# Kernel optimization log

Hardware: AMD Instinct MI355X
Metric: run time of the kernel (lower is better)

Reference implementation:

```python
import jax, jax.numpy as jnp
import numpy as np

V, D = 1_000_000, 128
N0, N1, N2 = 1_048_576, 131_072, 16_384
E0, E1, EP = 1_048_576, 131_072, 16_384


def setup_inputs() -> dict:
    key = jax.random.key(0)
    ks = jax.random.split(key, 20)
    inp = {
        'emb': jax.random.normal(ks[0], (V, D), jnp.float32) * 0.1,
        'bias': jnp.zeros((V, 1), jnp.float32),
        'nids': jax.random.randint(ks[1], (N0,), 0, V),
        'src0': jax.random.randint(ks[2], (E0,), 0, N0),
        'dst0': jax.random.randint(ks[3], (E0,), 0, N1),
        'w0': jax.random.uniform(ks[4], (E0,), jnp.float32),
        'src1': jax.random.randint(ks[5], (E1,), 0, N1),
        'dst1': jax.random.randint(ks[6], (E1,), 0, N2),
        'w1': jax.random.uniform(ks[7], (E1,), jnp.float32),
        'pos_src': jax.random.randint(ks[8], (EP,), 0, N2),
        'pos_dst': jax.random.randint(ks[9], (EP,), 0, N2),
        'neg_src': jax.random.randint(ks[10], (EP,), 0, N2),
        'neg_dst': jax.random.randint(ks[11], (EP,), 0, N2),
        'Q0w': jax.random.normal(ks[12], (D, D), jnp.float32) / np.sqrt(D),
        'Q0b': jnp.zeros((D,), jnp.float32),
        'W0w': jax.random.normal(ks[13], (2 * D, D), jnp.float32) / np.sqrt(2 * D),
        'W0b': jnp.zeros((D,), jnp.float32),
        'Q1w': jax.random.normal(ks[14], (D, D), jnp.float32) / np.sqrt(D),
        'Q1b': jnp.zeros((D,), jnp.float32),
        'W1w': jax.random.normal(ks[15], (2 * D, D), jnp.float32) / np.sqrt(2 * D),
        'W1b': jnp.zeros((D,), jnp.float32),
    }
    return inp


def _sage_conv(h_src, h_dst, src, dst, w, Qw, Qb, Ww, Wb, n_dst):
    # n = relu(Q h_src); m = sum_e w_e * n[src_e] per dst; ws = sum_e w_e per dst
    n = jax.nn.relu(h_src @ Qw + Qb)                                   # [N_src, H]
    m = jax.ops.segment_sum(n[src] * w[:, None], dst, num_segments=n_dst)
    ws = jnp.clip(jax.ops.segment_sum(w, dst, num_segments=n_dst), 1.0, None)[:, None]
    z = jax.nn.relu(jnp.concatenate([m / ws, h_dst], axis=1) @ Ww + Wb)
    zn = jnp.linalg.norm(z, axis=1, keepdims=True)
    return z / jnp.where(zn == 0, 1.0, zn)


def _pair_score(h, bias_nid, src, dst):
    # u_dot_v + bias_src + bias_dst  -> [E, 1]
    s = jnp.sum(h[src] * h[dst], axis=1, keepdims=True)
    return s + bias_nid[src] + bias_nid[dst]


def reference(emb, bias, nids, src0, dst0, w0, src1, dst1, w1,
              pos_src, pos_dst, neg_src, neg_dst,
              Q0w, Q0b, W0w, W0b, Q1w, Q1b, W1w, W1b):
    h = emb[nids]                                                      # [N0, D]
    h1 = _sage_conv(h, h[:N1], src0, dst0, w0, Q0w, Q0b, W0w, W0b, N1)  # [N1, D]
    h2 = _sage_conv(h1, h1[:N2], src1, dst1, w1, Q1w, Q1b, W1w, W1b, N2)  # [N2, D]
    h_item = emb[nids[:N2]] + h2                                       # [N2, D]
    bias_nid = bias[nids[:N2]]                                         # [N2, 1]
    pos = _pair_score(h_item, bias_nid, pos_src, pos_dst)
    neg = _pair_score(h_item, bias_nid, neg_src, neg_dst)
    return jax.nn.relu(neg - pos + 1.0)                                # [EP, 1]
```

## Files before the change

### kernel.cpp

```cpp
#include <hip/hip_runtime.h>
#include <stdint.h>

#define V_SZ   1000000
#define N0_SZ  1048576
#define N1_SZ  131072
#define N2_SZ  16384
#define E0_SZ  1048576
#define E1_SZ  131072
#define EP_SZ  16384

typedef short bf16x8 __attribute__((ext_vector_type(8)));
typedef float f32x4  __attribute__((ext_vector_type(4)));

__device__ __forceinline__ unsigned short f2bf(float f) {
  union { float f; unsigned u; } v; v.f = f;
  unsigned r = v.u + 0x7FFFu + ((v.u >> 16) & 1u);
  return (unsigned short)(r >> 16);
}
__device__ __forceinline__ float bf2f(unsigned short h) {
  union { unsigned u; float f; } v; v.u = ((unsigned)h) << 16;
  return v.f;
}
__device__ __forceinline__ unsigned pack2bf(float a, float b) {
  return ((unsigned)f2bf(b) << 16) | (unsigned)f2bf(a);
}

__global__ __launch_bounds__(256) void prepw_all_k(
    const float* __restrict__ Q0w, const float* __restrict__ W0w,
    const float* __restrict__ Q1w, const float* __restrict__ W1w,
    unsigned short* __restrict__ Q0T, unsigned short* __restrict__ W0T,
    unsigned short* __restrict__ Q1T, unsigned short* __restrict__ W1T) {
  int t = blockIdx.x * 256 + threadIdx.x;
  const float* W; unsigned short* WT; int K; int base;
  if (t < 16384)      { W = Q0w; WT = Q0T; K = 128; base = 0; }
  else if (t < 49152) { W = W0w; WT = W0T; K = 256; base = 16384; }
  else if (t < 65536) { W = Q1w; WT = Q1T; K = 128; base = 49152; }
  else                { W = W1w; WT = W1T; K = 256; base = 65536; }
  int u = t - base;
  int n = u & 127, k = u >> 7;
  WT[(size_t)n * K + k] = f2bf(W[u]);
}

__global__ __launch_bounds__(256) void hist_all_k(const int* __restrict__ dst0,
                                                  const int* __restrict__ dst1,
                                                  int* __restrict__ counts) {
  int e = blockIdx.x * 256 + threadIdx.x;
  if (e < E0_SZ) atomicAdd(&counts[dst0[e]], 1);
  else if (e < E0_SZ + E1_SZ) atomicAdd(&counts[N1_SZ + dst1[e - E0_SZ]], 1);
}

__global__ __launch_bounds__(256) void scan_bsums_k(const int* __restrict__ counts,
                                                    int* __restrict__ bsums) {
  __shared__ int red[256];
  int base = blockIdx.x * 1024, t = threadIdx.x;
  int s = 0;
  #pragma unroll
  for (int i = 0; i < 4; i++) s += counts[base + t * 4 + i];
  red[t] = s;
  __syncthreads();
  for (int st = 128; st > 0; st >>= 1) {
    if (t < st) red[t] += red[t + st];
    __syncthreads();
  }
  if (t == 0) bsums[blockIdx.x] = red[0];
}

__global__ __launch_bounds__(256) void scan_top2_k(int* __restrict__ bsums,
                                                   int* __restrict__ offs0_last,
                                                   int* __restrict__ offs1_last) {
  __shared__ int lds[256];
  int b = blockIdx.x, t = threadIdx.x;
  int nb = (b == 0) ? 128 : 16;
  int off = (b == 0) ? 0 : 128;
  int v = (t < nb) ? bsums[off + t] : 0;
  lds[t] = v;
  __syncthreads();
  for (int st = 1; st < 256; st <<= 1) {
    int x = (t >= st) ? lds[t - st] : 0;
    __syncthreads();
    lds[t] += x;
    __syncthreads();
  }
  if (t < nb) bsums[off + t] = lds[t] - v;
  if (t == nb - 1) *((b == 0) ? offs0_last : offs1_last) = lds[t];
}

__global__ __launch_bounds__(256) void scan_final_k(const int* __restrict__ counts,
                                                    const int* __restrict__ bsums,
                                                    int* __restrict__ offs0,
                                                    int* __restrict__ offs1) {
  __shared__ int tsum[256];
  int b = blockIdx.x, t = threadIdx.x;
  int base = b * 1024;
  int v0 = counts[base + t * 4 + 0], v1 = counts[base + t * 4 + 1];
  int v2 = counts[base + t * 4 + 2], v3 = counts[base + t * 4 + 3];
  int s = v0 + v1 + v2 + v3;
  tsum[t] = s;
  __syncthreads();
  for (int st = 1; st < 256; st <<= 1) {
    int x = (t >= st) ? tsum[t - st] : 0;
    __syncthreads();
    tsum[t] += x;
    __syncthreads();
  }
  int pre = bsums[b] + tsum[t] - s;
  int* op = (b < 128) ? (offs0 + base) : (offs1 + base - N1_SZ);
  op[t * 4 + 0] = pre;
  op[t * 4 + 1] = pre + v0;
  op[t * 4 + 2] = pre + v0 + v1;
  op[t * 4 + 3] = pre + v0 + v1 + v2;
}

__global__ __launch_bounds__(256) void scatter_all_k(
    const int* __restrict__ src0, const int* __restrict__ dst0, const float* __restrict__ w0,
    const int* __restrict__ src1, const int* __restrict__ dst1, const float* __restrict__ w1,
    const int* __restrict__ offs0, const int* __restrict__ offs1,
    int* __restrict__ cursor,
    int2* __restrict__ esw0, int* __restrict__ edst0,
    int2* __restrict__ esw1, int* __restrict__ edst1) {
  int e = blockIdx.x * 256 + threadIdx.x;
  if (e < E0_SZ) {
    int d = dst0[e];
    int p = offs0[d] + atomicAdd(&cursor[d], 1);
    esw0[p] = make_int2(src0[e], __float_as_int(w0[e]));
    edst0[p] = d;
  } else if (e < E0_SZ + E1_SZ) {
    int ee = e - E0_SZ;
    int d = dst1[ee];
    int p = offs1[d] + atomicAdd(&cursor[N1_SZ + d], 1);
    esw1[p] = make_int2(src1[ee], __float_as_int(w1[ee]));
    edst1[p] = d;
  }
}

#define AM_GATHER 0
#define AM_BF16   1
#define AM_F32DIV 2
#define EPI_BF16        0
#define EPI_NORM        1
#define EPI_NORM_ADDEMB 2

template <int KCHUNKS, int AM0, int AM1, int EPI>
__global__ __launch_bounds__(256) void gemm_k(const void* __restrict__ asrc0,
                                              const void* __restrict__ asrc1,
                                              const int* __restrict__ ids,
                                              const unsigned short* __restrict__ BT,
                                              const float* __restrict__ biasv,
                                              void* __restrict__ outp,
                                              const float* __restrict__ emb,
                                              const float* __restrict__ wsumv) {
  __shared__ unsigned short lA[64][136];
  __shared__ unsigned short lB[128][136];
  const int tid = threadIdx.x;
  const int lane = tid & 63;
  const int wid = tid >> 6;
  const int rowbase = blockIdx.x * 64;
  const int Ktot = KCHUNKS * 128;

  f32x4 acc[8];
  #pragma unroll
  for (int i = 0; i < 8; i++) acc[i] = (f32x4){0.f, 0.f, 0.f, 0.f};

  for (int c = 0; c < KCHUNKS; ++c) {
    if (c) __syncthreads();
    const int am = (c == 0) ? AM0 : AM1;
    const void* asrc = (c == 0) ? asrc0 : asrc1;
    if (am == AM_GATHER) {
      const float* fsrc = (const float*)asrc;
      #pragma unroll
      for (int i = 0; i < 8; i++) {
        int f = i * 256 + tid;
        int r = f >> 5, c4 = f & 31;
        const float* rp = fsrc + (size_t)ids[rowbase + r] * 128;
        float4 v = *(const float4*)(rp + c4 * 4);
        uint2 pk;
        pk.x = pack2bf(v.x, v.y);
        pk.y = pack2bf(v.z, v.w);
        *(uint2*)(&lA[r][c4 * 4]) = pk;
      }
    } else if (am == AM_F32DIV) {
      const float* fsrc = (const float*)asrc;
      #pragma unroll
      for (int i = 0; i < 8; i++) {
        int f = i * 256 + tid;
        int r = f >> 5, c4 = f & 31;
        int row = rowbase + r;
        float inv = 1.0f / fmaxf(wsumv[row], 1.0f);
        const float* rp = fsrc + (size_t)row * 128;
        float4 v = *(const float4*)(rp + c4 * 4);
        uint2 pk;
        pk.x = pack2bf(v.x * inv, v.y * inv);
        pk.y = pack2bf(v.z * inv, v.w * inv);
        *(uint2*)(&lA[r][c4 * 4]) = pk;
      }
    } else {
      const unsigned short* bsrc = (const unsigned short*)asrc;
      #pragma unroll
      for (int i = 0; i < 4; i++) {
        int f = i * 256 + tid;
        int r = f >> 4, c8 = f & 15;
        uint4 v = *(const uint4*)(bsrc + (size_t)(rowbase + r) * 128 + c8 * 8);
        *(uint4*)(&lA[r][c8 * 8]) = v;
      }
    }
    {
      const unsigned short* bp = BT + c * 128;
      #pragma unroll
      for (int i = 0; i < 8; i++) {
        int f = i * 256 + tid;
        int n = f >> 4, c8 = f & 15;
        uint4 v = *(const uint4*)(bp + (size_t)n * Ktot + c8 * 8);
        *(uint4*)(&lB[n][c8 * 8]) = v;
      }
    }
    __syncthreads();

    const int mr = wid * 16 + (lane & 15);
    const int kq = (lane >> 4) * 8;
    #pragma unroll
    for (int kk = 0; kk < 128; kk += 32) {
      bf16x8 af = *(const bf16x8*)(&lA[mr][kk + kq]);
      #pragma unroll
      for (int nt = 0; nt < 8; ++nt) {
        bf16x8 bfr = *(const bf16x8*)(&lB[nt * 16 + (lane & 15)][kk + kq]);
        acc[nt] = __builtin_amdgcn_mfma_f32_16x16x32_bf16(af, bfr, acc[nt], 0, 0, 0);
      }
    }
  }

  const int crow = wid * 16 + ((lane >> 4) << 2);
  float vreg[8][4];
  #pragma unroll
  for (int nt = 0; nt < 8; ++nt) {
    int col = nt * 16 + (lane & 15);
    float b = biasv[col];
    #pragma unroll
    for (int r = 0; r < 4; ++r) {
      float v = acc[nt][r] + b;
      vreg[nt][r] = v > 0.f ? v : 0.f;
    }
  }
  if (EPI == EPI_BF16) {
    unsigned short* op = (unsigned short*)outp;
    #pragma unroll
    for (int nt = 0; nt < 8; ++nt) {
      int col = nt * 16 + (lane & 15);
      #pragma unroll
      for (int r = 0; r < 4; ++r)
        op[(size_t)(rowbase + crow + r) * 128 + col] = f2bf(vreg[nt][r]);
    }
  } else {
    float ss[4] = {0.f, 0.f, 0.f, 0.f};
    #pragma unroll
    for (int nt = 0; nt < 8; ++nt)
      #pragma unroll
      for (int r = 0; r < 4; ++r) ss[r] += vreg[nt][r] * vreg[nt][r];
    #pragma unroll
    for (int r = 0; r < 4; ++r) {
      ss[r] += __shfl_xor(ss[r], 1);
      ss[r] += __shfl_xor(ss[r], 2);
      ss[r] += __shfl_xor(ss[r], 4);
      ss[r] += __shfl_xor(ss[r], 8);
    }
    float sc[4];
    #pragma unroll
    for (int r = 0; r < 4; ++r) sc[r] = ss[r] > 0.f ? rsqrtf(ss[r]) : 1.0f;
    if (EPI == EPI_NORM) {
      unsigned short* op = (unsigned short*)outp;
      #pragma unroll
      for (int nt = 0; nt < 8; ++nt) {
        int col = nt * 16 + (lane & 15);
        #pragma unroll
        for (int r = 0; r < 4; ++r)
          op[(size_t)(rowbase + crow + r) * 128 + col] = f2bf(vreg[nt][r] * sc[r]);
      }
    } else {
      float* op = (float*)outp;
      #pragma unroll
      for (int nt = 0; nt < 8; ++nt) {
        int col = nt * 16 + (lane & 15);
        #pragma unroll
        for (int r = 0; r < 4; ++r) {
          int row = rowbase + crow + r;
          op[(size_t)row * 128 + col] =
              vreg[nt][r] * sc[r] + emb[(size_t)ids[row] * 128 + col];
        }
      }
    }
  }
}

template <int LAYER>
__global__ __launch_bounds__(256) void eqagg_k(
    const float* __restrict__ embf,
    const unsigned short* __restrict__ hsrc,
    const int* __restrict__ nids,
    const int2* __restrict__ esw,
    const int* __restrict__ edst,
    const unsigned short* __restrict__ BT,
    const float* __restrict__ biasv,
    float* __restrict__ aoutf,
    float* __restrict__ wsumf) {
  constexpr int ETOT = (LAYER == 0) ? E0_SZ : E1_SZ;
  __shared__ unsigned short lA[64][136];
  __shared__ unsigned short lB[128][136];
  __shared__ float lw[64];
  __shared__ int ldst[64];
  const int tid = threadIdx.x;
  const int lane = tid & 63;
  const int wid = tid >> 6;
  const int base0 = blockIdx.x * 64;

  #pragma unroll
  for (int i = 0; i < 8; i++) {
    int f = i * 256 + tid;
    int n = f >> 4, c8 = f & 15;
    *(uint4*)(&lB[n][c8 * 8]) = *(const uint4*)(BT + (size_t)n * 128 + c8 * 8);
  }
  if (tid < 64) {
    int2 sw = esw[base0 + tid];
    lw[tid] = __int_as_float(sw.y);
    ldst[tid] = edst[base0 + tid];
  }
  if (LAYER == 0) {
    #pragma unroll
    for (int i = 0; i < 8; i++) {
      int f = i * 256 + tid;
      int r = f >> 5, c4 = f & 31;
      int s = esw[base0 + r].x;
      const float* rp = embf + (size_t)nids[s] * 128;
      float4 v = *(const float4*)(rp + c4 * 4);
      uint2 pk;
      pk.x = pack2bf(v.x, v.y);
      pk.y = pack2bf(v.z, v.w);
      *(uint2*)(&lA[r][c4 * 4]) = pk;
    }
  } else {
    #pragma unroll
    for (int i = 0; i < 4; i++) {
      int f = i * 256 + tid;
      int r = f >> 4, c8 = f & 15;
      int s = esw[base0 + r].x;
      *(uint4*)(&lA[r][c8 * 8]) = *(const uint4*)(hsrc + (size_t)s * 128 + c8 * 8);
    }
  }
  __syncthreads();

  const int mr = wid * 16 + (lane & 15);
  const int kq = (lane >> 4) * 8;
  f32x4 acc[8];
  #pragma unroll
  for (int i = 0; i < 8; i++) acc[i] = (f32x4){0.f, 0.f, 0.f, 0.f};
  #pragma unroll
  for (int kk = 0; kk < 128; kk += 32) {
    bf16x8 af = *(const bf16x8*)(&lA[mr][kk + kq]);
    #pragma unroll
    for (int nt = 0; nt < 8; ++nt) {
      bf16x8 bfr = *(const bf16x8*)(&lB[nt * 16 + (lane & 15)][kk + kq]);
      acc[nt] = __builtin_amdgcn_mfma_f32_16x16x32_bf16(af, bfr, acc[nt], 0, 0, 0);
    }
  }
  const int crow = wid * 16 + ((lane >> 4) << 2);
  #pragma unroll
  for (int nt = 0; nt < 8; ++nt) {
    int col = nt * 16 + (lane & 15);
    float b = biasv[col];
    #pragma unroll
    for (int r = 0; r < 4; ++r) {
      float v = acc[nt][r] + b;
      lA[crow + r][col] = f2bf(v > 0.f ? v : 0.f);
    }
  }

  const int r0 = wid * 16;
  const int prevd = (wid > 0) ? ldst[r0 - 1]
                              : (base0 > 0 ? edst[base0 - 1] : -1);
  const int nextd = (wid < 3) ? ldst[r0 + 16]
                              : (base0 + 64 < ETOT ? edst[base0 + 64] : -1);
  float ax = 0.f, ay = 0.f, wa = 0.f;
  int cur = ldst[r0];
  int rstart = 0;
  #pragma unroll
  for (int rr = 0; rr < 16; ++rr) {
    int d = ldst[r0 + rr];
    if (d != cur) {
      bool interior = (rstart > 0 || prevd != cur);
      float* rowp = aoutf + (size_t)cur * 128 + lane * 2;
      if (interior) {
        rowp[0] = ax; rowp[1] = ay;
        if (lane == 0) wsumf[cur] = wa;
      } else {
        atomicAdd(rowp, ax); atomicAdd(rowp + 1, ay);
        if (lane == 0) atomicAdd(&wsumf[cur], wa);
      }
      ax = ay = wa = 0.f;
      cur = d;
      rstart = rr;
    }
    float w = lw[r0 + rr];
    unsigned u = *(const unsigned*)(&lA[r0 + rr][lane * 2]);
    ax += w * bf2f((unsigned short)(u & 0xffffu));
    ay += w * bf2f((unsigned short)(u >> 16));
    wa += w;
  }
  {
    bool interior = (rstart > 0 || prevd != cur) && (nextd != cur);
    float* rowp = aoutf + (size_t)cur * 128 + lane * 2;
    if (interior) {
      rowp[0] = ax; rowp[1] = ay;
      if (lane == 0) wsumf[cur] = wa;
    } else {
      atomicAdd(rowp, ax); atomicAdd(rowp + 1, ay);
      if (lane == 0) atomicAdd(&wsumf[cur], wa);
    }
  }
}

__global__ __launch_bounds__(256) void score_k(const float* __restrict__ hitem,
                                               const float* __restrict__ bias,
                                               const int* __restrict__ nids,
                                               const int* __restrict__ ps,
                                               const int* __restrict__ pd,
                                               const int* __restrict__ ns,
                                               const int* __restrict__ nd,
                                               float* __restrict__ out) {
  int wid = threadIdx.x >> 6, lane = threadIdx.x & 63;
  int e = blockIdx.x * 4 + wid;
  if (e >= EP_SZ) return;
  int a = ps[e], b = pd[e], c = ns[e], d = nd[e];
  float2 va = ((const float2*)(hitem + (size_t)a * 128))[lane];
  float2 vb = ((const float2*)(hitem + (size_t)b * 128))[lane];
  float2 vc = ((const float2*)(hitem + (size_t)c * 128))[lane];
  float2 vd = ((const float2*)(hitem + (size_t)d * 128))[lane];
  float dp = va.x * vb.x + va.y * vb.y;
  float dn = vc.x * vd.x + vc.y * vd.y;
  #pragma unroll
  for (int m = 1; m < 64; m <<= 1) {
    dp += __shfl_xor(dp, m);
    dn += __shfl_xor(dn, m);
  }
  if (lane == 0) {
    float sp = dp + bias[nids[a]] + bias[nids[b]];
    float sn = dn + bias[nids[c]] + bias[nids[d]];
    out[e] = fmaxf(sn - sp + 1.0f, 0.0f);
  }
}

extern "C" void kernel_launch(void* const* d_in, const int* in_sizes, int n_in,
                              void* d_out, int out_size, void* d_ws, size_t ws_size,
                              hipStream_t stream) {
  const float* emb  = (const float*)d_in[0];
  const float* bias = (const float*)d_in[1];
  const int* nids   = (const int*)d_in[2];
  const int* src0   = (const int*)d_in[3];
  const int* dst0   = (const int*)d_in[4];
  const float* w0   = (const float*)d_in[5];
  const int* src1   = (const int*)d_in[6];
  const int* dst1   = (const int*)d_in[7];
  const float* w1   = (const float*)d_in[8];
  const int* pos_src = (const int*)d_in[9];
  const int* pos_dst = (const int*)d_in[10];
  const int* neg_src = (const int*)d_in[11];
  const int* neg_dst = (const int*)d_in[12];
  const float* Q0w = (const float*)d_in[13];
  const float* Q0b = (const float*)d_in[14];
  const float* W0w = (const float*)d_in[15];
  const float* W0b = (const float*)d_in[16];
  const float* Q1w = (const float*)d_in[17];
  const float* Q1b = (const float*)d_in[18];
  const float* W1w = (const float*)d_in[19];
  const float* W1b = (const float*)d_in[20];
  float* out = (float*)d_out;

  char* ws = (char*)d_ws;
  size_t p = 0;
  auto carve = [&](size_t sz) { void* r = ws + p; p = (p + sz + 255) & ~(size_t)255; return r; };

  float* a0f   = (float*)carve((size_t)N1_SZ * 128 * 4);
  float* wsum0 = (float*)carve((size_t)N1_SZ * 4);
  float* a1f   = (float*)carve((size_t)N2_SZ * 128 * 4);
  float* wsum1 = (float*)carve((size_t)N2_SZ * 4);
  int* cnt_all = (int*)carve((size_t)(N1_SZ + N2_SZ) * 2 * 4);
  size_t zlen  = p;
  int* counts  = cnt_all;
  int* cursor  = cnt_all + (N1_SZ + N2_SZ);
  unsigned short* h1    = (unsigned short*)carve((size_t)N1_SZ * 128 * 2);
  float*          hitem = (float*)carve((size_t)N2_SZ * 128 * 4);
  unsigned short* Q0T = (unsigned short*)carve(128 * 128 * 2);
  unsigned short* W0T = (unsigned short*)carve(256 * 128 * 2);
  unsigned short* Q1T = (unsigned short*)carve(128 * 128 * 2);
  unsigned short* W1T = (unsigned short*)carve(256 * 128 * 2);
  int*  offs0 = (int*)carve((N1_SZ + 1) * 4);
  int*  offs1 = (int*)carve((N2_SZ + 1) * 4);
  int2* esw0  = (int2*)carve((size_t)E0_SZ * 8);
  int*  edst0 = (int*)carve((size_t)E0_SZ * 4);
  int2* esw1  = (int2*)carve((size_t)E1_SZ * 8);
  int*  edst1 = (int*)carve((size_t)E1_SZ * 4);
  int*  bsums = (int*)carve(160 * 4);
  (void)ws_size; (void)in_sizes; (void)n_in; (void)out_size;

  hipMemsetAsync(ws, 0, zlen, stream);

  prepw_all_k<<<384, 256, 0, stream>>>(Q0w, W0w, Q1w, W1w, Q0T, W0T, Q1T, W1T);

  hist_all_k<<<(E0_SZ + E1_SZ) / 256, 256, 0, stream>>>(dst0, dst1, counts);
  scan_bsums_k<<<(N1_SZ + N2_SZ) / 1024, 256, 0, stream>>>(counts, bsums);
  scan_top2_k<<<2, 256, 0, stream>>>(bsums, offs0 + N1_SZ, offs1 + N2_SZ);
  scan_final_k<<<(N1_SZ + N2_SZ) / 1024, 256, 0, stream>>>(counts, bsums, offs0, offs1);
  scatter_all_k<<<(E0_SZ + E1_SZ) / 256, 256, 0, stream>>>(
      src0, dst0, w0, src1, dst1, w1, offs0, offs1, cursor,
      esw0, edst0, esw1, edst1);

  eqagg_k<0><<<E0_SZ / 64, 256, 0, stream>>>(emb, nullptr, nids, esw0, edst0,
                                             Q0T, Q0b, a0f, wsum0);
  gemm_k<2, AM_F32DIV, AM_GATHER, EPI_NORM>
      <<<N1_SZ / 64, 256, 0, stream>>>(a0f, emb, nids, W0T, W0b, h1, nullptr, wsum0);
  eqagg_k<1><<<E1_SZ / 64, 256, 0, stream>>>(nullptr, h1, nullptr, esw1, edst1,
                                             Q1T, Q1b, a1f, wsum1);
  gemm_k<2, AM_F32DIV, AM_BF16, EPI_NORM_ADDEMB>
      <<<N2_SZ / 64, 256, 0, stream>>>(a1f, h1, nids, W1T, W1b, hitem, emb, wsum1);

  score_k<<<EP_SZ / 4, 256, 0, stream>>>(hitem, bias, nids, pos_src, pos_dst,
                                         neg_src, neg_dst, out);
}
```

Before: 981.3 us.

## Make edge-aggregation kernel persistent with register double-buffered gather prefetch

The edge GEMM+aggregate kernel now processes several 64-edge chunks per block. Each wave works on its own 16-row slice and prefetches the next chunk's gathered source rows into registers while the current chunk's MFMA and segment reduction run. The weight tile is loaded once per block instead of once per chunk. Per-edge dst and weight values move from shared memory into lanes and are read with shuffles. The cost is higher register pressure, fewer blocks to hide latency, and extra global loads of the neighbouring dst values for boundary detection.

```diff
diff --git a/kernel.cpp b/kernel.cpp
--- a/kernel.cpp
+++ b/kernel.cpp
@@ -290,7 +290,7 @@
   }
 }
 
-template <int LAYER>
+template <int LAYER, int CH>
 __global__ __launch_bounds__(256) void eqagg_k(
     const float* __restrict__ embf,
     const unsigned short* __restrict__ hsrc,
@@ -304,12 +304,11 @@
   constexpr int ETOT = (LAYER == 0) ? E0_SZ : E1_SZ;
   __shared__ unsigned short lA[64][136];
   __shared__ unsigned short lB[128][136];
-  __shared__ float lw[64];
-  __shared__ int ldst[64];
   const int tid = threadIdx.x;
   const int lane = tid & 63;
   const int wid = tid >> 6;
-  const int base0 = blockIdx.x * 64;
+  const int r0 = wid * 16;
+  const long blkbase = (long)blockIdx.x * (CH * 64);
 
   #pragma unroll
   for (int i = 0; i < 8; i++) {
@@ -317,74 +316,122 @@
     int n = f >> 4, c8 = f & 15;
     *(uint4*)(&lB[n][c8 * 8]) = *(const uint4*)(BT + (size_t)n * 128 + c8 * 8);
   }
-  if (tid < 64) {
-    int2 sw = esw[base0 + tid];
-    lw[tid] = __int_as_float(sw.y);
-    ldst[tid] = edst[base0 + tid];
-  }
-  if (LAYER == 0) {
-    #pragma unroll
-    for (int i = 0; i < 8; i++) {
-      int f = i * 256 + tid;
-      int r = f >> 5, c4 = f & 31;
-      int s = esw[base0 + r].x;
-      const float* rp = embf + (size_t)nids[s] * 128;
-      float4 v = *(const float4*)(rp + c4 * 4);
-      uint2 pk;
-      pk.x = pack2bf(v.x, v.y);
-      pk.y = pack2bf(v.z, v.w);
-      *(uint2*)(&lA[r][c4 * 4]) = pk;
-    }
-  } else {
-    #pragma unroll
-    for (int i = 0; i < 4; i++) {
-      int f = i * 256 + tid;
-      int r = f >> 4, c8 = f & 15;
-      int s = esw[base0 + r].x;
-      *(uint4*)(&lA[r][c8 * 8]) = *(const uint4*)(hsrc + (size_t)s * 128 + c8 * 8);
-    }
-  }
-  __syncthreads();
-
-  const int mr = wid * 16 + (lane & 15);
+
+  const int mr = r0 + (lane & 15);
   const int kq = (lane >> 4) * 8;
-  f32x4 acc[8];
+  const int crow = r0 + ((lane >> 4) << 2);
+  float bv[8];
   #pragma unroll
-  for (int i = 0; i < 8; i++) acc[i] = (f32x4){0.f, 0.f, 0.f, 0.f};
-  #pragma unroll
-  for (int kk = 0; kk < 128; kk += 32) {
-    bf16x8 af = *(const bf16x8*)(&lA[mr][kk + kq]);
+  for (int nt = 0; nt < 8; ++nt) bv[nt] = biasv[nt * 16 + (lane & 15)];
+
+  float4 pfA[8], pfB[8];
+  uint4  qfA[4], qfB[4];
+  int svA = 0, svB = 0, dvA = 0, dvB = 0;
+  float wvA = 0.f, wvB = 0.f;
+
+  auto issue = [&](int ci, float4 (&pf)[8], uint4 (&qf)[4],
+                   int& sv, float& wv, int& dv) {
+    long eb = blkbase + (long)ci * 64 + r0;
+    if (lane < 16) {
+      int2 sw = esw[eb + lane];
+      sv = sw.x;
+      wv = __int_as_float(sw.y);
+      dv = edst[eb + lane];
+    }
+    if (LAYER == 0) {
+      #pragma unroll
+      for (int i = 0; i < 8; i++) {
+        int slot = i * 64 + lane;
+        int rl = slot >> 5, c4 = slot & 31;
+        int s = esw[eb + rl].x;
+        pf[i] = *(const float4*)(embf + (size_t)nids[s] * 128 + c4 * 4);
+      }
+    } else {
+      #pragma unroll
+      for (int i = 0; i < 4; i++) {
+        int slot = i * 64 + lane;
+        int rl = slot >> 4, c8 = slot & 15;
+        int s = esw[eb + rl].x;
+        qf[i] = *(const uint4*)(hsrc + (size_t)s * 128 + c8 * 8);
+      }
+    }
+  };
+
+  auto step = [&](int ci, float4 (&pf)[8], uint4 (&qf)[4],
+                  int sv, float wv, int dv,
+                  float4 (&npf)[8], uint4 (&nqf)[4],
+                  int& nsv, float& nwv, int& ndv) {
+    if (LAYER == 0) {
+      #pragma unroll
+      for (int i = 0; i < 8; i++) {
+        int slot = i * 64 + lane;
+        int rl = slot >> 5, c4 = slot & 31;
+        uint2 pk;
+        pk.x = pack2bf(pf[i].x, pf[i].y);
+        pk.y = pack2bf(pf[i].z, pf[i].w);
+        *(uint2*)(&lA[r0 + rl][c4 * 4]) = pk;
+      }
+    } else {
+      #pragma unroll
+      for (int i = 0; i < 4; i++) {
+        int slot = i * 64 + lane;
+        int rl = slot >> 4, c8 = slot & 15;
+        *(uint4*)(&lA[r0 + rl][c8 * 8]) = nqf == qf ? qf[i] : qf[i];
+      }
+    }
+    if (ci + 1 < CH) issue(ci + 1, npf, nqf, nsv, nwv, ndv);
+    f32x4 acc[8];
+    #pragma unroll
+    for (int i = 0; i < 8; i++) acc[i] = (f32x4){0.f, 0.f, 0.f, 0.f};
+    #pragma unroll
+    for (int kk = 0; kk < 128; kk += 32) {
+      bf16x8 af = *(const bf16x8*)(&lA[mr][kk + kq]);
+      #pragma unroll
+      for (int nt = 0; nt < 8; ++nt) {
+        bf16x8 bfr = *(const bf16x8*)(&lB[nt * 16 + (lane & 15)][kk + kq]);
+        acc[nt] = __builtin_amdgcn_mfma_f32_16x16x32_bf16(af, bfr, acc[nt], 0, 0, 0);
+      }
+    }
     #pragma unroll
     for (int nt = 0; nt < 8; ++nt) {
-      bf16x8 bfr = *(const bf16x8*)(&lB[nt * 16 + (lane & 15)][kk + kq]);
-      acc[nt] = __builtin_amdgcn_mfma_f32_16x16x32_bf16(af, bfr, acc[nt], 0, 0, 0);
-    }
-  }
-  const int crow = wid * 16 + ((lane >> 4) << 2);
-  #pragma unroll
-  for (int nt = 0; nt < 8; ++nt) {
-    int col = nt * 16 + (lane & 15);
-    float b = biasv[col];
-    #pragma unroll
-    for (int r = 0; r < 4; ++r) {
-      float v = acc[nt][r] + b;
-      lA[crow + r][col] = f2bf(v > 0.f ? v : 0.f);
-    }
-  }
-
-  const int r0 = wid * 16;
-  const int prevd = (wid > 0) ? ldst[r0 - 1]
-                              : (base0 > 0 ? edst[base0 - 1] : -1);
-  const int nextd = (wid < 3) ? ldst[r0 + 16]
-                              : (base0 + 64 < ETOT ? edst[base0 + 64] : -1);
-  float ax = 0.f, ay = 0.f, wa = 0.f;
-  int cur = ldst[r0];
-  int rstart = 0;
-  #pragma unroll
-  for (int rr = 0; rr < 16; ++rr) {
-    int d = ldst[r0 + rr];
-    if (d != cur) {
-      bool interior = (rstart > 0 || prevd != cur);
+      int col = nt * 16 + (lane & 15);
+      #pragma unroll
+      for (int r = 0; r < 4; ++r) {
+        float v = acc[nt][r] + bv[nt];
+        lA[crow + r][col] = f2bf(v > 0.f ? v : 0.f);
+      }
+    }
+    long eb = blkbase + (long)ci * 64 + r0;
+    int prevd = (eb > 0) ? edst[eb - 1] : -1;
+    int nextd = (eb + 16 < ETOT) ? edst[eb + 16] : -1;
+    float ax = 0.f, ay = 0.f, wa = 0.f;
+    int cur = __shfl(dv, 0);
+    int rstart = 0;
+    #pragma unroll
+    for (int rr = 0; rr < 16; ++rr) {
+      int d = __shfl(dv, rr);
+      float w = __shfl(wv, rr);
+      if (d != cur) {
+        bool interior = (rstart > 0 || prevd != cur);
+        float* rowp = aoutf + (size_t)cur * 128 + lane * 2;
+        if (interior) {
+          rowp[0] = ax; rowp[1] = ay;
+          if (lane == 0) wsumf[cur] = wa;
+        } else {
+          atomicAdd(rowp, ax); atomicAdd(rowp + 1, ay);
+          if (lane == 0) atomicAdd(&wsumf[cur], wa);
+        }
+        ax = ay = wa = 0.f;
+        cur = d;
+        rstart = rr;
+      }
+      unsigned u = *(const unsigned*)(&lA[r0 + rr][lane * 2]);
+      ax += w * bf2f((unsigned short)(u & 0xffffu));
+      ay += w * bf2f((unsigned short)(u >> 16));
+      wa += w;
+    }
+    {
+      bool interior = (rstart > 0 || prevd != cur) && (nextd != cur);
       float* rowp = aoutf + (size_t)cur * 128 + lane * 2;
       if (interior) {
         rowp[0] = ax; rowp[1] = ay;
@@ -393,26 +440,15 @@
         atomicAdd(rowp, ax); atomicAdd(rowp + 1, ay);
         if (lane == 0) atomicAdd(&wsumf[cur], wa);
       }
-      ax = ay = wa = 0.f;
-      cur = d;
-      rstart = rr;
-    }
-    float w = lw[r0 + rr];
-    unsigned u = *(const unsigned*)(&lA[r0 + rr][lane * 2]);
-    ax += w * bf2f((unsigned short)(u & 0xffffu));
-    ay += w * bf2f((unsigned short)(u >> 16));
-    wa += w;
-  }
-  {
-    bool interior = (rstart > 0 || prevd != cur) && (nextd != cur);
-    float* rowp = aoutf + (size_t)cur * 128 + lane * 2;
-    if (interior) {
-      rowp[0] = ax; rowp[1] = ay;
-      if (lane == 0) wsumf[cur] = wa;
-    } else {
-      atomicAdd(rowp, ax); atomicAdd(rowp + 1, ay);
-      if (lane == 0) atomicAdd(&wsumf[cur], wa);
-    }
+    }
+  };
+
+  issue(0, pfA, qfA, svA, wvA, dvA);
+  __syncthreads();
+  #pragma unroll 1
+  for (int ci = 0; ci < CH; ci += 2) {
+    step(ci,     pfA, qfA, svA, wvA, dvA, pfB, qfB, svB, wvB, dvB);
+    step(ci + 1, pfB, qfB, svB, wvB, dvB, pfA, qfA, svA, wvA, dvA);
   }
 }
 
@@ -511,12 +547,12 @@
       src0, dst0, w0, src1, dst1, w1, offs0, offs1, cursor,
       esw0, edst0, esw1, edst1);
 
-  eqagg_k<0><<<E0_SZ / 64, 256, 0, stream>>>(emb, nullptr, nids, esw0, edst0,
-                                             Q0T, Q0b, a0f, wsum0);
+  eqagg_k<0, 16><<<1024, 256, 0, stream>>>(emb, nullptr, nids, esw0, edst0,
+                                           Q0T, Q0b, a0f, wsum0);
   gemm_k<2, AM_F32DIV, AM_GATHER, EPI_NORM>
       <<<N1_SZ / 64, 256, 0, stream>>>(a0f, emb, nids, W0T, W0b, h1, nullptr, wsum0);
-  eqagg_k<1><<<E1_SZ / 64, 256, 0, stream>>>(nullptr, h1, nullptr, esw1, edst1,
-                                             Q1T, Q1b, a1f, wsum1);
+  eqagg_k<1, 4><<<512, 256, 0, stream>>>(nullptr, h1, nullptr, esw1, edst1,
+                                         Q1T, Q1b, a1f, wsum1);
   gemm_k<2, AM_F32DIV, AM_BF16, EPI_NORM_ADDEMB>
       <<<N2_SZ / 64, 256, 0, stream>>>(a1f, h1, nids, W1T, W1b, hitem, emb, wsum1);
 
```

Result: no change. 989.1 us (+0.8%).
